# Kernel tuning notes

Measured on AMD Instinct MI355X. Metric: run time of the kernel, lower is better.

## Reference

```python
import jax, jax.numpy as jnp
import numpy as np

NEG_INF = -1.0e12  # matches masked_fill value in the torch module


def _entmax15(x, axis=-1):
    """Exact entmax with alpha=1.5 (Peters & Martins, 2019), sort-based."""
    x = x - jnp.max(x, axis=axis, keepdims=True)
    x = x / 2.0
    d = x.shape[axis]
    xs = -jnp.sort(-x, axis=axis)  # descending sort along normalization axis
    rho = jnp.arange(1, d + 1, dtype=x.dtype)  # 1..d, broadcasts on last axis
    mean = jnp.cumsum(xs, axis=axis) / rho
    mean_sq = jnp.cumsum(xs * xs, axis=axis) / rho
    ss = rho * (mean_sq - mean * mean)
    delta = (1.0 - ss) / rho
    tau = mean - jnp.sqrt(jnp.clip(delta, 0.0))
    support = jnp.sum((tau <= xs).astype(jnp.int32), axis=axis, keepdims=True)
    tau_star = jnp.take_along_axis(tau, support - 1, axis=axis)
    y = jnp.clip(x - tau_star, 0.0)
    return y * y


def setup_inputs() -> dict:
    key = jax.random.key(0)
    kq, kk, kv, km = jax.random.split(key, 4)
    B, H, S, D = 4, 8, 1024, 128
    q = jax.random.normal(kq, (B, H, S, D), dtype=jnp.float32)
    k = jax.random.normal(kk, (B, H, S, D), dtype=jnp.float32)
    v = jax.random.normal(kv, (B, H, S, D), dtype=jnp.float32)
    mask = jax.random.randint(km, (B, 1, S, S), 0, 2, dtype=jnp.int32)
    return {"q": q, "k": k, "v": v, "mask": mask}


def reference(q, k, v, mask):
    D = q.shape[-1]
    scale = 1.0 / jnp.sqrt(jnp.asarray(D, dtype=q.dtype))
    scores = jnp.einsum("bhqd,bhkd->bhqk", q, k) * scale
    scores = jnp.where(mask == 0, jnp.asarray(NEG_INF, dtype=scores.dtype), scores)
    attn = _entmax15(scores, axis=-1)
    return jnp.einsum("bhqk,bhkd->bhqd", attn, v)
```

## Files before the change

kernel.cpp:

```cpp
#include <hip/hip_runtime.h>


#define S_ 1024
#define D_ 128
#define NEG_INF_F (-1.0e12f)
#define SCALE_F 0.08838834764831845f
#define NITER 26
#define SCP 1028

typedef float f32x4 __attribute__((ext_vector_type(4)));
typedef short short8 __attribute__((ext_vector_type(8)));

__device__ __forceinline__ ushort f2bf(float x) {
    unsigned u = __builtin_bit_cast(unsigned, x);
    u += 0x7FFFu + ((u >> 16) & 1u);
    return (ushort)(u >> 16);
}
__device__ __forceinline__ float bf2f(ushort h) {
    unsigned u = ((unsigned)h) << 16;
    return __builtin_bit_cast(float, u);
}

__global__ void cvt_k(const float* __restrict__ K, ushort* __restrict__ Kb) {
    int i = blockIdx.x * 256 + threadIdx.x;
    float4 v = ((const float4*)K)[i];
    ushort4 o; o.x = f2bf(v.x); o.y = f2bf(v.y); o.z = f2bf(v.z); o.w = f2bf(v.w);
    ((ushort4*)Kb)[i] = o;
}

__global__ void cvt_vT(const float* __restrict__ V, ushort* __restrict__ Vt) {
    __shared__ ushort tile[128][132];
    const int bh = blockIdx.x >> 3, kt = blockIdx.x & 7;
    const int t = threadIdx.x;
    const float4* src = (const float4*)(V + ((size_t)(bh * S_ + kt * 128)) * D_);
    #pragma unroll
    for (int u = 0; u < 16; ++u) {
        int i = t + u * 256;
        int r = i >> 5, c = i & 31;
        float4 v = src[r * 32 + c];
        ushort4 o; o.x = f2bf(v.x); o.y = f2bf(v.y); o.z = f2bf(v.z); o.w = f2bf(v.w);
        *(ushort4*)&tile[r][c * 4] = o;
    }
    __syncthreads();
    const int d = t >> 1, h = t & 1;
    ushort* dst = Vt + ((size_t)(bh * D_ + d)) * S_ + kt * 128 + h * 64;
    #pragma unroll
    for (int jj = 0; jj < 8; ++jj) {
        short8 val;
        #pragma unroll
        for (int e = 0; e < 8; ++e)
            ((ushort*)&val)[e] = tile[h * 64 + jj * 8 + e][d];
        *(short8*)(dst + jj * 8) = val;
    }
}

__global__ __launch_bounds__(512, 4)
void entmax_attn(const float* __restrict__ Q, const ushort* __restrict__ Kb,
                 const ushort* __restrict__ Vt, const int* __restrict__ M,
                 float* __restrict__ O)
{
    __shared__ __align__(16) ushort sc[16][SCP];
    __shared__ __align__(16) ushort kv[128][136];
    __shared__ __align__(16) ushort q_s[16][136];

    const int t = threadIdx.x;
    const int w = t >> 6, lane = t & 63, l = lane & 15, quad = lane >> 4;
    const int bh = blockIdx.x >> 6, qt = blockIdx.x & 63, b = bh >> 3;

    const ushort* kb_bh = Kb + (size_t)bh * S_ * D_;
    const ushort* vt_bh = Vt + (size_t)bh * D_ * S_;

    int cr[4], cc[4];
    #pragma unroll
    for (int i = 0; i < 4; ++i) {
        int cell = t + i * 512;
        cr[i] = cell >> 4; cc[i] = cell & 15;
    }

    {
        const float4* qsrc = (const float4*)(Q + ((size_t)bh * S_ + (size_t)qt * 16) * D_);
        int r = t >> 5, c = t & 31;
        float4 v = qsrc[r * 32 + c];
        ushort4 o;
        o.x = f2bf(v.x); o.y = f2bf(v.y); o.z = f2bf(v.z); o.w = f2bf(v.w);
        *(ushort4*)&q_s[r][c * 4] = o;
    }
    short8 sreg[4];
    #pragma unroll
    for (int i = 0; i < 4; ++i)
        sreg[i] = *(const short8*)(kb_bh + (size_t)cr[i] * D_ + cc[i] * 8);

    __syncthreads();

    short8 aq[4];
    #pragma unroll
    for (int ks = 0; ks < 4; ++ks)
        aq[ks] = *(const short8*)&q_s[l][ks * 32 + quad * 8];

    #pragma unroll
    for (int i = 0; i < 4; ++i) *(short8*)&kv[cr[i]][cc[i] * 8] = sreg[i];
    __syncthreads();

    #pragma unroll 1
    for (int kt = 0; kt < 8; ++kt) {
        if (kt < 7) {
            const ushort* nb = kb_bh + (size_t)(kt + 1) * 128 * D_;
            #pragma unroll
            for (int i = 0; i < 4; ++i)
                sreg[i] = *(const short8*)(nb + (size_t)cr[i] * D_ + cc[i] * 8);
        }
        f32x4 acc = {0.f, 0.f, 0.f, 0.f};
        const int n = w * 16 + l;
        #pragma unroll
        for (int ks = 0; ks < 4; ++ks) {
            short8 bk = *(const short8*)&kv[n][ks * 32 + quad * 8];
            acc = __builtin_amdgcn_mfma_f32_16x16x32_bf16(aq[ks], bk, acc, 0, 0, 0);
        }
        #pragma unroll
        for (int r = 0; r < 4; ++r)
            sc[quad * 4 + r][kt * 128 + w * 16 + l] = f2bf(acc[r] * SCALE_F);
        __syncthreads();
        if (kt < 7) {
            #pragma unroll
            for (int i = 0; i < 4; ++i) *(short8*)&kv[cr[i]][cc[i] * 8] = sreg[i];
            __syncthreads();
        }
    }

    #pragma unroll
    for (int i = 0; i < 4; ++i)
        sreg[i] = *(const short8*)(vt_bh + (size_t)cr[i] * S_ + cc[i] * 8);

    const int row = t >> 5, u = t & 31;
    const int qg = qt * 16 + row;
    float x[32];
    #pragma unroll
    for (int c = 0; c < 4; ++c) {
        short8 v8 = *(const short8*)&sc[row][c * 256 + u * 8];
        #pragma unroll
        for (int e = 0; e < 8; ++e) x[c * 8 + e] = bf2f(((ushort*)&v8)[e]);
    }
    {
        const int4* mrow = (const int4*)(M + ((size_t)b * S_ + qg) * S_);
        #pragma unroll
        for (int c = 0; c < 4; ++c) {
            #pragma unroll
            for (int h = 0; h < 2; ++h) {
                int4 mm = mrow[c * 64 + u * 2 + h];
                if (mm.x == 0) x[c * 8 + h * 4 + 0] = NEG_INF_F;
                if (mm.y == 0) x[c * 8 + h * 4 + 1] = NEG_INF_F;
                if (mm.z == 0) x[c * 8 + h * 4 + 2] = NEG_INF_F;
                if (mm.w == 0) x[c * 8 + h * 4 + 3] = NEG_INF_F;
            }
        }
    }
    float mx = -3.0e38f;
    #pragma unroll
    for (int j = 0; j < 32; ++j) mx = fmaxf(mx, x[j]);
    #pragma unroll
    for (int off = 1; off < 32; off <<= 1) mx = fmaxf(mx, __shfl_xor(mx, off));
    #pragma unroll
    for (int j = 0; j < 32; ++j) x[j] = (x[j] - mx) * 0.5f;

    float lo = -1.f, hi = 0.f;
    #pragma unroll 1
    for (int it = 0; it < NITER; ++it) {
        const float tau = 0.5f * (lo + hi);
        float f = 0.f;
        #pragma unroll
        for (int j = 0; j < 32; ++j) {
            float d = fmaxf(x[j] - tau, 0.f);
            f = fmaf(d, d, f);
        }
        #pragma unroll
        for (int off = 1; off < 32; off <<= 1) f += __shfl_xor(f, off);
        const bool ge = (f >= 1.f);
        lo = ge ? tau : lo;
        hi = ge ? hi : tau;
    }
    const float tau = 0.5f * (lo + hi);

    #pragma unroll
    for (int c = 0; c < 4; ++c) {
        short8 v8;
        #pragma unroll
        for (int e = 0; e < 8; ++e) {
            float d = fmaxf(x[c * 8 + e] - tau, 0.f);
            ((ushort*)&v8)[e] = f2bf(d * d);
        }
        *(short8*)&sc[row][c * 256 + u * 8] = v8;
    }
    #pragma unroll
    for (int i = 0; i < 4; ++i) *(short8*)&kv[cr[i]][cc[i] * 8] = sreg[i];
    __syncthreads();

    f32x4 oa = {0.f, 0.f, 0.f, 0.f};
    #pragma unroll 1
    for (int vt = 0; vt < 8; ++vt) {
        if (vt < 7) {
            const ushort* nb = vt_bh + (size_t)(vt + 1) * 128;
            #pragma unroll
            for (int i = 0; i < 4; ++i)
                sreg[i] = *(const short8*)(nb + (size_t)cr[i] * S_ + cc[i] * 8);
        }
        const int d = w * 16 + l;
        #pragma unroll
        for (int ki = 0; ki < 4; ++ki) {
            short8 ap = *(const short8*)&sc[l][vt * 128 + ki * 32 + quad * 8];
            short8 bv = *(const short8*)&kv[d][ki * 32 + quad * 8];
            oa = __builtin_amdgcn_mfma_f32_16x16x32_bf16(ap, bv, oa, 0, 0, 0);
        }
        __syncthreads();
        if (vt < 7) {
            #pragma unroll
            for (int i = 0; i < 4; ++i) *(short8*)&kv[cr[i]][cc[i] * 8] = sreg[i];
            __syncthreads();
        }
    }

    float* ob = O + ((size_t)bh * S_ + (size_t)qt * 16) * D_;
    #pragma unroll
    for (int r = 0; r < 4; ++r)
        ob[(size_t)(quad * 4 + r) * D_ + w * 16 + l] = oa[r];
}

extern "C" void kernel_launch(void* const* d_in, const int* in_sizes, int n_in,
                              void* d_out, int out_size, void* d_ws, size_t ws_size,
                              hipStream_t stream) {
    const float* q = (const float*)d_in[0];
    const float* k = (const float*)d_in[1];
    const float* v = (const float*)d_in[2];
    const int*   m = (const int*)d_in[3];
    float*       o = (float*)d_out;

    ushort* Kb = (ushort*)d_ws;
    ushort* Vt = (ushort*)((char*)d_ws + 8388608);

    cvt_k <<<4096, 256, 0, stream>>>(k, Kb);
    cvt_vT<<<256, 256, 0, stream>>>(v, Vt);
    entmax_attn<<<2048, 512, 0, stream>>>(q, Kb, Vt, m, o);
}
```

Measured before the change: 214.1 us.

## Compact entmax candidates above threshold and fuse K/V conversion kernels

Before bisection, each row's scores greater than -1 (the only entries that can be in the entmax support, since tau lies in [-1,0]) are compacted into shared memory using ballot and mbcnt. The bisection then iterates only over these candidates, and a fallback keeps the full-register path when a row has more than 512 candidates. The iteration count drops from 26 to 14, which gives a coarser tau. The K conversion and the V transpose-conversion are merged into one launch with smaller transpose tiles, and an extra barrier protects the candidate buffer, which reuses the kv shared memory.

After: 204.4 us. -4.5%, faster.

```diff
diff --git a/kernel.cpp b/kernel.cpp
--- a/kernel.cpp
+++ b/kernel.cpp
@@ -5,8 +5,10 @@
 #define D_ 128
 #define NEG_INF_F (-1.0e12f)
 #define SCALE_F 0.08838834764831845f
-#define NITER 26
+#define NITER 14
 #define SCP 1028
+#define CCAP 512
+#define CSTR 516
 
 typedef float f32x4 __attribute__((ext_vector_type(4)));
 typedef short short8 __attribute__((ext_vector_type(8)));
@@ -21,36 +23,40 @@
     return __builtin_bit_cast(float, u);
 }
 
-__global__ void cvt_k(const float* __restrict__ K, ushort* __restrict__ Kb) {
-    int i = blockIdx.x * 256 + threadIdx.x;
-    float4 v = ((const float4*)K)[i];
-    ushort4 o; o.x = f2bf(v.x); o.y = f2bf(v.y); o.z = f2bf(v.z); o.w = f2bf(v.w);
-    ((ushort4*)Kb)[i] = o;
-}
-
-__global__ void cvt_vT(const float* __restrict__ V, ushort* __restrict__ Vt) {
-    __shared__ ushort tile[128][132];
-    const int bh = blockIdx.x >> 3, kt = blockIdx.x & 7;
+__global__ __launch_bounds__(256)
+void pre_cvt(const float* __restrict__ K, const float* __restrict__ V,
+             ushort* __restrict__ Kb, ushort* __restrict__ Vt)
+{
+    __shared__ ushort tile[64][72];
     const int t = threadIdx.x;
-    const float4* src = (const float4*)(V + ((size_t)(bh * S_ + kt * 128)) * D_);
-    #pragma unroll
-    for (int u = 0; u < 16; ++u) {
-        int i = t + u * 256;
-        int r = i >> 5, c = i & 31;
-        float4 v = src[r * 32 + c];
-        ushort4 o; o.x = f2bf(v.x); o.y = f2bf(v.y); o.z = f2bf(v.z); o.w = f2bf(v.w);
+    if (blockIdx.x < 4096) {
+        int i = blockIdx.x * 256 + t;
+        float4 v = ((const float4*)K)[i];
+        ushort4 o;
+        o.x = f2bf(v.x); o.y = f2bf(v.y); o.z = f2bf(v.z); o.w = f2bf(v.w);
+        ((ushort4*)Kb)[i] = o;
+        return;
+    }
+    const int vb = blockIdx.x - 4096;
+    const int bh = vb >> 5, r5 = vb & 31, kt = r5 >> 1, dh = r5 & 1;
+    const float* src = V + ((size_t)(bh * S_ + kt * 64)) * D_ + dh * 64;
+    #pragma unroll
+    for (int i = 0; i < 4; ++i) {
+        int idx = t + i * 256, r = idx >> 4, c = idx & 15;
+        float4 vv = *(const float4*)(src + (size_t)r * D_ + c * 4);
+        ushort4 o;
+        o.x = f2bf(vv.x); o.y = f2bf(vv.y); o.z = f2bf(vv.z); o.w = f2bf(vv.w);
         *(ushort4*)&tile[r][c * 4] = o;
     }
     __syncthreads();
-    const int d = t >> 1, h = t & 1;
-    ushort* dst = Vt + ((size_t)(bh * D_ + d)) * S_ + kt * 128 + h * 64;
-    #pragma unroll
-    for (int jj = 0; jj < 8; ++jj) {
-        short8 val;
-        #pragma unroll
-        for (int e = 0; e < 8; ++e)
-            ((ushort*)&val)[e] = tile[h * 64 + jj * 8 + e][d];
-        *(short8*)(dst + jj * 8) = val;
+    ushort* dst = Vt + ((size_t)(bh * D_ + dh * 64)) * S_ + kt * 64;
+    #pragma unroll
+    for (int i = 0; i < 2; ++i) {
+        int idx = t + i * 256, d = idx >> 3, jj = idx & 7;
+        short8 val; ushort* vp = (ushort*)&val;
+        #pragma unroll
+        for (int e = 0; e < 8; ++e) vp[e] = tile[jj * 8 + e][d];
+        *(short8*)(dst + (size_t)d * S_ + jj * 8) = val;
     }
 }
 
@@ -162,23 +168,61 @@
     #pragma unroll
     for (int j = 0; j < 32; ++j) x[j] = (x[j] - mx) * 0.5f;
 
-    float lo = -1.f, hi = 0.f;
-    #pragma unroll 1
-    for (int it = 0; it < NITER; ++it) {
-        const float tau = 0.5f * (lo + hi);
-        float f = 0.f;
-        #pragma unroll
-        for (int j = 0; j < 32; ++j) {
-            float d = fmaxf(x[j] - tau, 0.f);
-            f = fmaf(d, d, f);
-        }
-        #pragma unroll
-        for (int off = 1; off < 32; off <<= 1) f += __shfl_xor(f, off);
-        const bool ge = (f >= 1.f);
-        lo = ge ? tau : lo;
-        hi = ge ? hi : tau;
-    }
-    const float tau = 0.5f * (lo + hi);
+    float* cand = (float*)&kv[0][0];
+    const unsigned long long halfmask =
+        (lane >= 32) ? 0xFFFFFFFF00000000ull : 0x00000000FFFFFFFFull;
+    int cnt = 0;
+    #pragma unroll
+    for (int j = 0; j < 32; ++j) {
+        const bool p = (x[j] > -1.0f);
+        unsigned long long bal = __ballot(p) & halfmask;
+        if (p) {
+            int pos = cnt + (int)__builtin_amdgcn_mbcnt_hi(
+                (unsigned)(bal >> 32),
+                __builtin_amdgcn_mbcnt_lo((unsigned)bal, 0));
+            if (pos < CCAP) cand[row * CSTR + pos] = x[j];
+        }
+        cnt += __popcll(bal);
+    }
+
+    float tau;
+    if (cnt <= CCAP) {
+        const float* crow = cand + row * CSTR;
+        float lo = -1.f, hi = 0.f;
+        #pragma unroll 1
+        for (int it = 0; it < NITER; ++it) {
+            const float tm = 0.5f * (lo + hi);
+            float f = 0.f;
+            for (int j = u; j < cnt; j += 32) {
+                float d = fmaxf(crow[j] - tm, 0.f);
+                f = fmaf(d, d, f);
+            }
+            #pragma unroll
+            for (int off = 1; off < 32; off <<= 1) f += __shfl_xor(f, off);
+            const bool ge = (f >= 1.f);
+            lo = ge ? tm : lo;
+            hi = ge ? hi : tm;
+        }
+        tau = 0.5f * (lo + hi);
+    } else {
+        float lo = -1.f, hi = 0.f;
+        #pragma unroll 1
+        for (int it = 0; it < NITER; ++it) {
+            const float tm = 0.5f * (lo + hi);
+            float f = 0.f;
+            #pragma unroll
+            for (int j = 0; j < 32; ++j) {
+                float d = fmaxf(x[j] - tm, 0.f);
+                f = fmaf(d, d, f);
+            }
+            #pragma unroll
+            for (int off = 1; off < 32; off <<= 1) f += __shfl_xor(f, off);
+            const bool ge = (f >= 1.f);
+            lo = ge ? tm : lo;
+            hi = ge ? hi : tm;
+        }
+        tau = 0.5f * (lo + hi);
+    }
 
     #pragma unroll
     for (int c = 0; c < 4; ++c) {
@@ -190,6 +234,7 @@
         }
         *(short8*)&sc[row][c * 256 + u * 8] = v8;
     }
+    __syncthreads();
     #pragma unroll
     for (int i = 0; i < 4; ++i) *(short8*)&kv[cr[i]][cc[i] * 8] = sreg[i];
     __syncthreads();
@@ -236,7 +281,6 @@
     ushort* Kb = (ushort*)d_ws;
     ushort* Vt = (ushort*)((char*)d_ws + 8388608);
 
-    cvt_k <<<4096, 256, 0, stream>>>(k, Kb);
-    cvt_vT<<<256, 256, 0, stream>>>(v, Vt);
+    pre_cvt<<<5120, 256, 0, stream>>>(k, v, Kb, Vt);
     entmax_attn<<<2048, 512, 0, stream>>>(q, Kb, Vt, m, o);
 }
```
